# Kernel optimization log

Measured on AMD Instinct MI355X. Metric: run time of the kernel, lower is better.

The kernel has to match this reference:

```python
import jax, jax.numpy as jnp
import numpy as np

B, S, D, H, E = 4, 2048, 1024, 4096, 8
TOP_K = 2


def setup_inputs() -> dict:
    key = jax.random.key(0)
    k = jax.random.split(key, 7)
    scale_in = 1.0 / np.sqrt(D)
    scale_h = 1.0 / np.sqrt(H)
    return {
        "x": jax.random.normal(k[0], (B, S, D), jnp.float32),
        "Wr": jax.random.normal(k[1], (D, E), jnp.float32) * scale_in,
        "br": jnp.zeros((E,), jnp.float32),
        "W1": jax.random.normal(k[2], (E, D, H), jnp.float32) * scale_in,
        "b1": jnp.zeros((E, H), jnp.float32),
        "W2": jax.random.normal(k[3], (E, H, D), jnp.float32) * scale_h,
        "b2": jnp.zeros((E, D), jnp.float32),
    }


def reference(x, Wr, br, W1, b1, W2, b2):
    # Router: softmax over experts, then top-k and renormalize.
    routing = jax.nn.softmax(x @ Wr + br, axis=-1)            # [B,S,E]
    topk_vals, topk_idx = jax.lax.top_k(routing, TOP_K)        # [B,S,K]
    topk_norm = topk_vals / jnp.sum(topk_vals, axis=-1, keepdims=True)
    # Scatter normalized top-k weights back to a dense [B,S,E] gate.
    gate = jnp.sum(jax.nn.one_hot(topk_idx, E, dtype=x.dtype) * topk_norm[..., None], axis=2)  # [B,S,E]
    # Per-expert FFN over all tokens (original's dense masked loop; masked-out
    # tokens have gate==0 so zeroing inputs is mathematically equivalent).
    h = jax.nn.relu(jnp.einsum("bsd,edh->ebsh", x, W1) + b1[:, None, None, :])  # [E,B,S,H]
    y = jnp.einsum("ebsh,ehd->ebsd", h, W2) + b2[:, None, None, :]              # [E,B,S,D]
    out = jnp.einsum("ebsd,bse->bsd", y, gate)                                   # [B,S,D]
    return out
```

## Files before the change

### kernel.cpp

```cpp
#include <hip/hip_runtime.h>
#include <stdint.h>

typedef unsigned short u16;
typedef __attribute__((ext_vector_type(8))) short s8bf;
typedef __attribute__((ext_vector_type(4))) float f32x4;

#define N_TOK 8192
#define DIM   1024
#define HID   4096
#define NE    8
#define MAX_SLOTS 17408
#define MAX_TILES 160
#define TSTR  264
#define LSTR  152

#define OFF_W1T  ((size_t)0)
#define OFF_Y    ((size_t)0)
#define OFF_W2T  ((size_t)67108864)
#define OFF_XB   ((size_t)134217728)
#define OFF_H    ((size_t)150994944)
#define OFF_TOS  ((size_t)293601280)
#define OFF_SOT  ((size_t)293670912)
#define OFF_TKI  ((size_t)293740544)
#define OFF_TKW  ((size_t)293806080)
#define OFF_CNT  ((size_t)293871616)
#define OFF_POF  ((size_t)293871680)
#define OFF_CUR  ((size_t)293871744)
#define OFF_NT   ((size_t)293871808)
#define OFF_TE   ((size_t)293871872)
#define OFF_TS   ((size_t)293872896)

__device__ __forceinline__ u16 f2b(float v) {
  union { float f; uint32_t u; } c; c.f = v;
  uint32_t u = c.u;
  return (u16)((u + 0x7FFFu + ((u >> 16) & 1u)) >> 16);
}
__device__ __forceinline__ float b2f(u16 b) {
  union { uint32_t u; float f; } c; c.u = ((uint32_t)b) << 16; return c.f;
}

typedef const __attribute__((address_space(1))) uint32_t* gp32;
typedef __attribute__((address_space(3))) uint32_t* lp32;
__device__ __forceinline__ void gl_lds16(const u16* g, u16* l) {
  __builtin_amdgcn_global_load_lds((gp32)(const void*)g, (lp32)(void*)l, 16, 0, 0);
}

__global__ __launch_bounds__(256) void transpose_to_bf16(
    const float* __restrict__ in, u16* __restrict__ out, int R, int C) {
  __shared__ u16 L[64 * TSTR];
  int tiles_c = C >> 6, tiles_r = R >> 8;
  int per = tiles_c * tiles_r;
  int e = blockIdx.x / per, t = blockIdx.x % per;
  int tr = t / tiles_c, tc = t % tiles_c;
  const float* ip = in + (size_t)e * R * C + (size_t)(tr * 256) * C + tc * 64;
  u16* op = out + (size_t)e * R * C + (size_t)(tc * 64) * R + tr * 256;
  const int tid = threadIdx.x;
  const int c = tid & 63;
  const int rb0 = (tid >> 6) * 8;
  #pragma unroll
  for (int p = 0; p < 8; p++) {
    int rb = p * 32 + rb0;
    u16 tmp[8];
    #pragma unroll
    for (int j = 0; j < 8; j++) tmp[j] = f2b(ip[(size_t)(rb + j) * C + c]);
    *(uint4*)&L[c * TSTR + rb] = *(const uint4*)tmp;
  }
  __syncthreads();
  const int s = tid & 31, ocb = tid >> 5;
  #pragma unroll
  for (int p = 0; p < 8; p++) {
    int oc = p * 8 + ocb;
    uint4 v = *(const uint4*)&L[oc * TSTR + s * 8];
    *(uint4*)&op[(size_t)oc * R + s * 8] = v;
  }
}

__global__ __launch_bounds__(256) void convert_x(const float* __restrict__ x,
                                                 u16* __restrict__ xb) {
  size_t i = ((size_t)blockIdx.x * 256 + threadIdx.x) * 8;
  float4 v0 = *(const float4*)(x + i);
  float4 v1 = *(const float4*)(x + i + 4);
  u16 o[8] = {f2b(v0.x), f2b(v0.y), f2b(v0.z), f2b(v0.w),
              f2b(v1.x), f2b(v1.y), f2b(v1.z), f2b(v1.w)};
  *(uint4*)(xb + i) = *(const uint4*)o;
}

__global__ __launch_bounds__(256) void router_kernel(
    const float* __restrict__ x, const float* __restrict__ Wr,
    const float* __restrict__ br, int* __restrict__ tki, float* __restrict__ tkw,
    int* __restrict__ counts) {
  int wave = threadIdx.x >> 6, lane = threadIdx.x & 63;
  int t = blockIdx.x * 4 + wave;
  const float* xr = x + (size_t)t * DIM;
  float acc[8] = {0.f, 0.f, 0.f, 0.f, 0.f, 0.f, 0.f, 0.f};
  #pragma unroll
  for (int i = 0; i < 16; i++) {
    int d = lane + i * 64;
    float xv = xr[d];
    float4 wa = *(const float4*)(Wr + d * 8);
    float4 wb = *(const float4*)(Wr + d * 8 + 4);
    acc[0] += xv * wa.x; acc[1] += xv * wa.y; acc[2] += xv * wa.z; acc[3] += xv * wa.w;
    acc[4] += xv * wb.x; acc[5] += xv * wb.y; acc[6] += xv * wb.z; acc[7] += xv * wb.w;
  }
  #pragma unroll
  for (int e = 0; e < 8; e++)
    #pragma unroll
    for (int off = 32; off >= 1; off >>= 1)
      acc[e] += __shfl_xor(acc[e], off, 64);
  if (lane == 0) {
    float l[8];
    #pragma unroll
    for (int e = 0; e < 8; e++) l[e] = acc[e] + br[e];
    float l0 = -1e30f; int i0 = 0;
    #pragma unroll
    for (int e = 0; e < 8; e++) if (l[e] > l0) { l0 = l[e]; i0 = e; }
    float l1 = -1e30f; int i1 = 0;
    #pragma unroll
    for (int e = 0; e < 8; e++) if (e != i0 && l[e] > l1) { l1 = l[e]; i1 = e; }
    float w0 = 1.f / (1.f + expf(l1 - l0));
    tki[t * 2] = i0; tki[t * 2 + 1] = i1;
    tkw[t * 2] = w0; tkw[t * 2 + 1] = 1.f - w0;
    atomicAdd(&counts[i0], 1);
    atomicAdd(&counts[i1], 1);
  }
}

__global__ void plan_kernel(const int* __restrict__ counts, int* __restrict__ poff,
                            int* __restrict__ cursor, int* __restrict__ ntiles,
                            int* __restrict__ tile_e, int* __restrict__ tile_s0) {
  int e = threadIdx.x;
  if (e < NE) {
    int po = 0, tb = 0;
    for (int i = 0; i < e; i++) {
      int tl = (counts[i] + 127) >> 7;
      po += tl << 7; tb += tl;
    }
    poff[e] = po;
    cursor[e] = 0;
    int tl = (counts[e] + 127) >> 7;
    for (int j = 0; j < tl; j++) { tile_e[tb + j] = e; tile_s0[tb + j] = po + j * 128; }
    if (e == NE - 1) ntiles[0] = tb + tl;
  }
}

__global__ __launch_bounds__(256) void scatter_kernel(
    const int* __restrict__ tki, const int* __restrict__ poff,
    int* __restrict__ cursor, int* __restrict__ token_of_slot,
    int* __restrict__ slot_of_token) {
  int t = blockIdx.x * 256 + threadIdx.x;
  #pragma unroll
  for (int k = 0; k < 2; k++) {
    int e = tki[t * 2 + k];
    int r = atomicAdd(&cursor[e], 1);
    int s = poff[e] + r;
    token_of_slot[s] = t;
    slot_of_token[t * 2 + k] = s;
  }
}

template <int MODE>
__global__ __launch_bounds__(256, 2) void moe_gemm(
    const u16* __restrict__ A, const u16* __restrict__ Bt,
    const float* __restrict__ bias, u16* __restrict__ Hout,
    const int* __restrict__ tile_e, const int* __restrict__ tile_s0,
    const int* __restrict__ ntiles, const int* __restrict__ token_of_slot,
    int K, int N, int NB) {
  __shared__ u16 SM[32768];

  const int nblk = blockIdx.x % NB;
  const int tileid = blockIdx.x / NB;
  if (tileid >= ntiles[0]) return;
  const int e = tile_e[tileid];
  const int slot0 = tile_s0[tileid];
  const int n0 = nblk * 128;
  const int T = K >> 6;

  const int tid = threadIdx.x;
  const int lane = tid & 63;
  const int wave = tid >> 6;
  const int wm = wave >> 1;
  const int wn = wave & 1;

  const int srow = tid >> 3;
  const int sslot = tid & 7;
  const u16* aB[4];
  const u16* bB[4];
  #pragma unroll
  for (int s = 0; s < 4; s++) {
    int row = s * 32 + srow;
    int scol = (sslot ^ (row & 7)) * 8;
    int arow;
    if (MODE == 1) { int t0 = token_of_slot[slot0 + row]; arow = t0 < 0 ? 0 : t0; }
    else arow = slot0 + row;
    aB[s] = A + (size_t)arow * K + scol;
  }
  const u16* bE = Bt + (size_t)e * N * K;
  #pragma unroll
  for (int s = 0; s < 4; s++) {
    int row = s * 32 + srow;
    int scol = (sslot ^ (row & 7)) * 8;
    bB[s] = bE + (size_t)(n0 + row) * K + scol;
  }

  const int colq = lane & 15;
  float bv[4];
  #pragma unroll
  for (int n = 0; n < 4; n++) bv[n] = bias[(size_t)e * N + n0 + wn * 64 + n * 16 + colq];
  asm volatile("s_waitcnt vmcnt(0)" ::: "memory");

  const int wo = wave * 512;
  #pragma unroll
  for (int tt = 0; tt < 2; tt++) {
    const int kq = tt * 64;
    u16* LA = SM + tt * 8192;
    u16* LB = SM + 16384 + tt * 8192;
    #pragma unroll
    for (int s = 0; s < 4; s++) gl_lds16(aB[s] + kq, LA + s * 2048 + wo);
    #pragma unroll
    for (int s = 0; s < 4; s++) gl_lds16(bB[s] + kq, LB + s * 2048 + wo);
  }
  asm volatile("s_waitcnt vmcnt(8)" ::: "memory");
  __builtin_amdgcn_s_barrier();

  const int q4 = lane >> 4;
  const int sx = lane & 7;
  const int sk0 = (q4 ^ sx) * 8;
  const int sk1 = sk0 ^ 32;
  const int aOff = (wm * 64 + (lane & 15)) * 64;
  const int bOff = (wn * 64 + (lane & 15)) * 64;

  f32x4 acc[4][4];
  #pragma unroll
  for (int i = 0; i < 4; i++)
    #pragma unroll
    for (int j = 0; j < 4; j++) acc[i][j] = (f32x4){0.f, 0.f, 0.f, 0.f};

  int kk = 128;
  for (int t = 0; t < T; ++t) {
    const int cb = t & 1;
    const u16* LA = SM + cb * 8192;
    const u16* LB = SM + 16384 + cb * 8192;
    u16* sLA = SM + cb * 8192;
    u16* sLB = SM + 16384 + cb * 8192;
    s8bf af[4][2], bf[4][2];

    #pragma unroll
    for (int m = 0; m < 4; m++) {
      af[m][0] = *(const s8bf*)&LA[aOff + m * 1024 + sk0];
      af[m][1] = *(const s8bf*)&LA[aOff + m * 1024 + sk1];
    }
    #pragma unroll
    for (int n = 0; n < 2; n++) {
      bf[n][0] = *(const s8bf*)&LB[bOff + n * 1024 + sk0];
      bf[n][1] = *(const s8bf*)&LB[bOff + n * 1024 + sk1];
    }
    __builtin_amdgcn_sched_barrier(0);
    __builtin_amdgcn_s_barrier();
    __builtin_amdgcn_s_setprio(1);
    #pragma unroll
    for (int ks = 0; ks < 2; ks++)
      #pragma unroll
      for (int m = 0; m < 4; m++)
        #pragma unroll
        for (int n = 0; n < 2; n++)
          acc[m][n] = __builtin_amdgcn_mfma_f32_16x16x32_bf16(af[m][ks], bf[n][ks],
                                                              acc[m][n], 0, 0, 0);
    __builtin_amdgcn_s_setprio(0);
    __builtin_amdgcn_s_barrier();

    #pragma unroll
    for (int n = 2; n < 4; n++) {
      bf[n][0] = *(const s8bf*)&LB[bOff + n * 1024 + sk0];
      bf[n][1] = *(const s8bf*)&LB[bOff + n * 1024 + sk1];
    }
    __builtin_amdgcn_sched_barrier(0);
    __builtin_amdgcn_s_barrier();
    __builtin_amdgcn_s_setprio(1);
    #pragma unroll
    for (int ks = 0; ks < 2; ks++)
      #pragma unroll
      for (int m = 0; m < 4; m++)
        #pragma unroll
        for (int n = 2; n < 4; n++)
          acc[m][n] = __builtin_amdgcn_mfma_f32_16x16x32_bf16(af[m][ks], bf[n][ks],
                                                              acc[m][n], 0, 0, 0);
    __builtin_amdgcn_s_setprio(0);
    asm volatile("s_waitcnt lgkmcnt(0)" ::: "memory");
    __builtin_amdgcn_sched_barrier(0);
    __builtin_amdgcn_s_barrier();

    if (t + 2 < T) {
      #pragma unroll
      for (int s = 0; s < 4; s++) gl_lds16(aB[s] + kk, sLA + s * 2048 + wo);
      #pragma unroll
      for (int s = 0; s < 4; s++) gl_lds16(bB[s] + kk, sLB + s * 2048 + wo);
    }
    __builtin_amdgcn_sched_barrier(0);
    if (t < T - 2)       asm volatile("s_waitcnt vmcnt(8)" ::: "memory");
    else if (t == T - 2) asm volatile("s_waitcnt vmcnt(0)" ::: "memory");
    if (t < T - 1) {
      __builtin_amdgcn_sched_barrier(0);
      __builtin_amdgcn_s_barrier();
    }
    kk += 64;
  }

  __syncthreads();
  const int rq = (lane >> 4) * 4;
  #pragma unroll
  for (int nt = 0; nt < 4; nt++) {
    int lcol = wn * 64 + nt * 16 + colq;
    #pragma unroll
    for (int mt = 0; mt < 4; mt++) {
      int rowbase = wm * 64 + mt * 16 + rq;
      #pragma unroll
      for (int r = 0; r < 4; r++) {
        float v = acc[mt][nt][r] + bv[nt];
        if (MODE == 1) v = fmaxf(v, 0.f);
        SM[(rowbase + r) * LSTR + lcol] = f2b(v);
      }
    }
  }
  __syncthreads();
  #pragma unroll
  for (int k = 0; k < 8; k++) {
    int ch = k * 256 + tid;
    int row = ch >> 4;
    int cp = (ch & 15) * 8;
    uint4 v = *(const uint4*)&SM[row * LSTR + cp];
    *(uint4*)&Hout[(size_t)(slot0 + row) * N + n0 + cp] = v;
  }
}

__global__ __launch_bounds__(256) void combine_kernel(
    const u16* __restrict__ y, const int* __restrict__ sot,
    const float* __restrict__ tkw, float* __restrict__ out) {
  int wave = threadIdx.x >> 6, lane = threadIdx.x & 63;
  int t = blockIdx.x * 4 + wave;
  int s0 = sot[t * 2], s1 = sot[t * 2 + 1];
  float w0 = tkw[t * 2], w1 = tkw[t * 2 + 1];
  const u16* y0 = y + (size_t)s0 * DIM;
  const u16* y1 = y + (size_t)s1 * DIM;
  float* op = out + (size_t)t * DIM;
  #pragma unroll
  for (int i = 0; i < 4; i++) {
    int d = i * 256 + lane * 4;
    uint2 a = *(const uint2*)(y0 + d);
    uint2 b = *(const uint2*)(y1 + d);
    float4 o;
    o.x = w0 * b2f((u16)(a.x & 0xFFFF)) + w1 * b2f((u16)(b.x & 0xFFFF));
    o.y = w0 * b2f((u16)(a.x >> 16))    + w1 * b2f((u16)(b.x >> 16));
    o.z = w0 * b2f((u16)(a.y & 0xFFFF)) + w1 * b2f((u16)(b.y & 0xFFFF));
    o.w = w0 * b2f((u16)(a.y >> 16))    + w1 * b2f((u16)(b.y >> 16));
    *(float4*)(op + d) = o;
  }
}

extern "C" void kernel_launch(void* const* d_in, const int* in_sizes, int n_in,
                              void* d_out, int out_size, void* d_ws, size_t ws_size,
                              hipStream_t stream) {
  const float* x  = (const float*)d_in[0];
  const float* Wr = (const float*)d_in[1];
  const float* br = (const float*)d_in[2];
  const float* W1 = (const float*)d_in[3];
  const float* b1 = (const float*)d_in[4];
  const float* W2 = (const float*)d_in[5];
  const float* b2 = (const float*)d_in[6];
  float* out = (float*)d_out;
  char* ws = (char*)d_ws;

  u16*   W1t  = (u16*)(ws + OFF_W1T);
  u16*   W2t  = (u16*)(ws + OFF_W2T);
  u16*   ybuf = (u16*)(ws + OFF_Y);
  u16*   xb   = (u16*)(ws + OFF_XB);
  u16*   hbuf = (u16*)(ws + OFF_H);
  int*   tos  = (int*)(ws + OFF_TOS);
  int*   sot  = (int*)(ws + OFF_SOT);
  int*   tki  = (int*)(ws + OFF_TKI);
  float* tkw  = (float*)(ws + OFF_TKW);
  int*   cnt  = (int*)(ws + OFF_CNT);
  int*   pof  = (int*)(ws + OFF_POF);
  int*   cur  = (int*)(ws + OFF_CUR);
  int*   nt   = (int*)(ws + OFF_NT);
  int*   te   = (int*)(ws + OFF_TE);
  int*   ts   = (int*)(ws + OFF_TS);

  hipMemsetAsync(tos, 0xFF, (size_t)MAX_SLOTS * sizeof(int), stream);
  hipMemsetAsync(cnt, 0, 8 * sizeof(int), stream);

  transpose_to_bf16<<<dim3(NE * (DIM / 256) * (HID / 64)), 256, 0, stream>>>(W1, W1t, DIM, HID);
  transpose_to_bf16<<<dim3(NE * (HID / 256) * (DIM / 64)), 256, 0, stream>>>(W2, W2t, HID, DIM);
  convert_x<<<dim3(N_TOK * DIM / (256 * 8)), 256, 0, stream>>>(x, xb);
  router_kernel<<<dim3(N_TOK / 4), 256, 0, stream>>>(x, Wr, br, tki, tkw, cnt);
  plan_kernel<<<dim3(1), 64, 0, stream>>>(cnt, pof, cur, nt, te, ts);
  scatter_kernel<<<dim3(N_TOK / 256), 256, 0, stream>>>(tki, pof, cur, tos, sot);

  moe_gemm<1><<<dim3((MAX_SLOTS / 128) * (HID / 128)), 256, 0, stream>>>(
      xb, W1t, b1, hbuf, te, ts, nt, tos, DIM, HID, HID / 128);
  moe_gemm<2><<<dim3((MAX_SLOTS / 128) * (DIM / 128)), 256, 0, stream>>>(
      hbuf, W2t, b2, ybuf, te, ts, nt, tos, HID, DIM, DIM / 128);
  combine_kernel<<<dim3(N_TOK / 4), 256, 0, stream>>>(ybuf, sot, tkw, out);
}
```

Before: 959.4 us.

## Vectorize weight transpose, fuse x conversion into router, batch scatter atomics

The weight transpose now reads float4 vectors per thread instead of scalar strided loads, with a new LDS stride. The fp32-to-bf16 conversion of x moves into the router kernel, which already reads x, removing one kernel and one full pass over x. The token_of_slot memset is replaced by filling only the padding slots inside plan_kernel, and scatter uses per-block LDS counters with one global atomic per expert. Together these cut launches and memory traffic in the preprocessing stages, but the router now issues 2-byte scalar stores and slot ordering within an expert changes.

Measured after the change: 886.9 us. 1.08x faster.

```diff
diff --git a/kernel.cpp b/kernel.cpp
--- a/kernel.cpp
+++ b/kernel.cpp
@@ -11,7 +11,7 @@
 #define NE    8
 #define MAX_SLOTS 17408
 #define MAX_TILES 160
-#define TSTR  264
+#define T2STR 272
 #define LSTR  152
 
 #define OFF_W1T  ((size_t)0)
@@ -47,7 +47,7 @@
 
 __global__ __launch_bounds__(256) void transpose_to_bf16(
     const float* __restrict__ in, u16* __restrict__ out, int R, int C) {
-  __shared__ u16 L[64 * TSTR];
+  __shared__ u16 L[64 * T2STR];
   int tiles_c = C >> 6, tiles_r = R >> 8;
   int per = tiles_c * tiles_r;
   int e = blockIdx.x / per, t = blockIdx.x % per;
@@ -55,48 +55,56 @@
   const float* ip = in + (size_t)e * R * C + (size_t)(tr * 256) * C + tc * 64;
   u16* op = out + (size_t)e * R * C + (size_t)(tc * 64) * R + tr * 256;
   const int tid = threadIdx.x;
-  const int c = tid & 63;
-  const int rb0 = (tid >> 6) * 8;
-  #pragma unroll
-  for (int p = 0; p < 8; p++) {
-    int rb = p * 32 + rb0;
-    u16 tmp[8];
-    #pragma unroll
-    for (int j = 0; j < 8; j++) tmp[j] = f2b(ip[(size_t)(rb + j) * C + c]);
-    *(uint4*)&L[c * TSTR + rb] = *(const uint4*)tmp;
-  }
-  __syncthreads();
-  const int s = tid & 31, ocb = tid >> 5;
-  #pragma unroll
-  for (int p = 0; p < 8; p++) {
-    int oc = p * 8 + ocb;
-    uint4 v = *(const uint4*)&L[oc * TSTR + s * 8];
-    *(uint4*)&op[(size_t)oc * R + s * 8] = v;
-  }
-}
-
-__global__ __launch_bounds__(256) void convert_x(const float* __restrict__ x,
-                                                 u16* __restrict__ xb) {
-  size_t i = ((size_t)blockIdx.x * 256 + threadIdx.x) * 8;
-  float4 v0 = *(const float4*)(x + i);
-  float4 v1 = *(const float4*)(x + i + 4);
-  u16 o[8] = {f2b(v0.x), f2b(v0.y), f2b(v0.z), f2b(v0.w),
-              f2b(v1.x), f2b(v1.y), f2b(v1.z), f2b(v1.w)};
-  *(uint4*)(xb + i) = *(const uint4*)o;
+
+  const int c4 = (tid & 15) * 4;
+  const int rq = (tid >> 4) * 4;
+  #pragma unroll
+  for (int p = 0; p < 4; p++) {
+    int r0 = p * 64 + rq;
+    float4 v0 = *(const float4*)(ip + (size_t)(r0 + 0) * C + c4);
+    float4 v1 = *(const float4*)(ip + (size_t)(r0 + 1) * C + c4);
+    float4 v2 = *(const float4*)(ip + (size_t)(r0 + 2) * C + c4);
+    float4 v3 = *(const float4*)(ip + (size_t)(r0 + 3) * C + c4);
+    const float* f0 = (const float*)&v0;
+    const float* f1 = (const float*)&v1;
+    const float* f2 = (const float*)&v2;
+    const float* f3 = (const float*)&v3;
+    #pragma unroll
+    for (int i = 0; i < 4; i++) {
+      u16 w[4] = {f2b(f0[i]), f2b(f1[i]), f2b(f2[i]), f2b(f3[i])};
+      *(uint2*)&L[(c4 + i) * T2STR + r0] = *(const uint2*)w;
+    }
+  }
+  __syncthreads();
+
+  const int oc0 = tid >> 4;
+  const int ch  = tid & 15;
+  #pragma unroll
+  for (int jr = 0; jr < 4; jr++) {
+    int oc = jr * 16 + oc0;
+    #pragma unroll
+    for (int h = 0; h < 2; h++) {
+      int co = (ch + h * 16) * 8;
+      uint4 v = *(const uint4*)&L[oc * T2STR + co];
+      *(uint4*)&op[(size_t)oc * R + co] = v;
+    }
+  }
 }
 
 __global__ __launch_bounds__(256) void router_kernel(
     const float* __restrict__ x, const float* __restrict__ Wr,
-    const float* __restrict__ br, int* __restrict__ tki, float* __restrict__ tkw,
-    int* __restrict__ counts) {
+    const float* __restrict__ br, u16* __restrict__ xb,
+    int* __restrict__ tki, float* __restrict__ tkw, int* __restrict__ counts) {
   int wave = threadIdx.x >> 6, lane = threadIdx.x & 63;
   int t = blockIdx.x * 4 + wave;
   const float* xr = x + (size_t)t * DIM;
+  u16* xo = xb + (size_t)t * DIM;
   float acc[8] = {0.f, 0.f, 0.f, 0.f, 0.f, 0.f, 0.f, 0.f};
   #pragma unroll
   for (int i = 0; i < 16; i++) {
     int d = lane + i * 64;
     float xv = xr[d];
+    xo[d] = f2b(xv);
     float4 wa = *(const float4*)(Wr + d * 8);
     float4 wb = *(const float4*)(Wr + d * 8 + 4);
     acc[0] += xv * wa.x; acc[1] += xv * wa.y; acc[2] += xv * wa.z; acc[3] += xv * wa.w;
@@ -127,9 +135,12 @@
 
 __global__ void plan_kernel(const int* __restrict__ counts, int* __restrict__ poff,
                             int* __restrict__ cursor, int* __restrict__ ntiles,
-                            int* __restrict__ tile_e, int* __restrict__ tile_s0) {
-  int e = threadIdx.x;
-  if (e < NE) {
+                            int* __restrict__ tile_e, int* __restrict__ tile_s0,
+                            int* __restrict__ tos) {
+  __shared__ int spo[NE], scnt[NE];
+  int tid = threadIdx.x;
+  if (tid < NE) {
+    int e = tid;
     int po = 0, tb = 0;
     for (int i = 0; i < e; i++) {
       int tl = (counts[i] + 127) >> 7;
@@ -137,9 +148,16 @@
     }
     poff[e] = po;
     cursor[e] = 0;
+    spo[e] = po; scnt[e] = counts[e];
     int tl = (counts[e] + 127) >> 7;
     for (int j = 0; j < tl; j++) { tile_e[tb + j] = e; tile_s0[tb + j] = po + j * 128; }
     if (e == NE - 1) ntiles[0] = tb + tl;
+  }
+  __syncthreads();
+  for (int e = 0; e < NE; e++) {
+    int start = spo[e] + scnt[e];
+    int end = spo[e] + (((scnt[e] + 127) >> 7) << 7);
+    for (int i = start + tid; i < end; i += 64) tos[i] = -1;
   }
 }
 
@@ -147,15 +165,23 @@
     const int* __restrict__ tki, const int* __restrict__ poff,
     int* __restrict__ cursor, int* __restrict__ token_of_slot,
     int* __restrict__ slot_of_token) {
+  __shared__ int lcnt[NE], lbase[NE];
+  if (threadIdx.x < NE) lcnt[threadIdx.x] = 0;
+  __syncthreads();
   int t = blockIdx.x * 256 + threadIdx.x;
-  #pragma unroll
-  for (int k = 0; k < 2; k++) {
-    int e = tki[t * 2 + k];
-    int r = atomicAdd(&cursor[e], 1);
-    int s = poff[e] + r;
-    token_of_slot[s] = t;
-    slot_of_token[t * 2 + k] = s;
-  }
+  int e0 = tki[t * 2], e1 = tki[t * 2 + 1];
+  int r0 = atomicAdd(&lcnt[e0], 1);
+  int r1 = atomicAdd(&lcnt[e1], 1);
+  __syncthreads();
+  if (threadIdx.x < NE)
+    lbase[threadIdx.x] = atomicAdd(&cursor[threadIdx.x], lcnt[threadIdx.x]);
+  __syncthreads();
+  int s0 = poff[e0] + lbase[e0] + r0;
+  int s1 = poff[e1] + lbase[e1] + r1;
+  token_of_slot[s0] = t;
+  token_of_slot[s1] = t;
+  slot_of_token[t * 2] = s0;
+  slot_of_token[t * 2 + 1] = s1;
 }
 
 template <int MODE>
@@ -385,14 +411,12 @@
   int*   te   = (int*)(ws + OFF_TE);
   int*   ts   = (int*)(ws + OFF_TS);
 
-  hipMemsetAsync(tos, 0xFF, (size_t)MAX_SLOTS * sizeof(int), stream);
   hipMemsetAsync(cnt, 0, 8 * sizeof(int), stream);
 
   transpose_to_bf16<<<dim3(NE * (DIM / 256) * (HID / 64)), 256, 0, stream>>>(W1, W1t, DIM, HID);
   transpose_to_bf16<<<dim3(NE * (HID / 256) * (DIM / 64)), 256, 0, stream>>>(W2, W2t, HID, DIM);
-  convert_x<<<dim3(N_TOK * DIM / (256 * 8)), 256, 0, stream>>>(x, xb);
-  router_kernel<<<dim3(N_TOK / 4), 256, 0, stream>>>(x, Wr, br, tki, tkw, cnt);
-  plan_kernel<<<dim3(1), 64, 0, stream>>>(cnt, pof, cur, nt, te, ts);
+  router_kernel<<<dim3(N_TOK / 4), 256, 0, stream>>>(x, Wr, br, xb, tki, tkw, cnt);
+  plan_kernel<<<dim3(1), 64, 0, stream>>>(cnt, pof, cur, nt, te, ts, tos);
   scatter_kernel<<<dim3(N_TOK / 256), 256, 0, stream>>>(tki, pof, cur, tos, sot);
 
   moe_gemm<1><<<dim3((MAX_SLOTS / 128) * (HID / 128)), 256, 0, stream>>>(
```
